# Performance work log

Hardware: AMD Instinct MI355X
Metric: run time of the kernel (lower is better)

The kernel has to match this reference:

```python
import jax, jax.numpy as jnp
import numpy as np

B, S, HIDDEN = 2, 2048, 2048
H, KVH, HD = 16, 4, 128
N_REP = H // KVH
WIN = 3  # hardcoded window_size in the module
ROPE_THETA = 10000.0


def _rope(x, cos, sin):
    # x: [b, s, h, d]; cos/sin: [s, d//2]. Pairs are consecutive elements
    # (view_as_complex on reshape(..., -1, 2)): a = even idx, b = odd idx.
    a = x[..., 0::2]
    b = x[..., 1::2]
    c = cos[None, :, None, :]
    s = sin[None, :, None, :]
    out = jnp.stack([a * c - b * s, a * s + b * c], axis=-1)  # [b,s,h,d//2,2]
    return out.reshape(x.shape)


def setup_inputs() -> dict:
    key = jax.random.key(0)
    ks = jax.random.split(key, 5)
    x = jax.random.normal(ks[0], (B, S, HIDDEN), dtype=jnp.float32)
    scale = 0.02
    wq = jax.random.normal(ks[1], (HIDDEN, H * HD), dtype=jnp.float32) * scale
    wk = jax.random.normal(ks[2], (HIDDEN, KVH * HD), dtype=jnp.float32) * scale
    wv = jax.random.normal(ks[3], (HIDDEN, KVH * HD), dtype=jnp.float32) * scale
    wo = jax.random.normal(ks[4], (H * HD, HIDDEN), dtype=jnp.float32) * scale
    # Standard RoPE angles (equivalent to the complex freqs_cis)
    inv_freq = 1.0 / (ROPE_THETA ** (np.arange(0, HD, 2, dtype=np.float64) / HD))
    ang = np.outer(np.arange(S, dtype=np.float64), inv_freq)  # [S, HD//2]
    cos = jnp.asarray(np.cos(ang), dtype=jnp.float32)
    sin = jnp.asarray(np.sin(ang), dtype=jnp.float32)
    return {"x": x, "wq": wq, "wk": wk, "wv": wv, "wo": wo, "cos": cos, "sin": sin}


def reference(x, wq, wk, wv, wo, cos, sin):
    q = (x @ wq).reshape(B, S, H, HD)
    k = (x @ wk).reshape(B, S, KVH, HD)
    v = (x @ wv).reshape(B, S, KVH, HD)
    q = _rope(q, cos, sin)
    k = _rope(k, cos, sin)
    # GQA: repeat kv heads (repeat_kv)
    k = jnp.repeat(k, N_REP, axis=2)  # [B,S,H,HD]
    v = jnp.repeat(v, N_REP, axis=2)
    scores = jnp.einsum("bqhd,bkhd->bhqk", q, k) / np.float32(np.sqrt(HD))
    i = jnp.arange(S)[:, None]
    j = jnp.arange(S)[None, :]
    allowed = (j <= i) & (j > i - WIN)
    scores = jnp.where(allowed, scores, -jnp.inf)
    attn = jax.nn.softmax(scores.astype(jnp.float32), axis=-1).astype(q.dtype)
    out = jnp.einsum("bhqk,bkhd->bqhd", attn, v).reshape(B, S, H * HD)
    return (out @ wo, attn)
```

## Files before the change

kernel.cpp:

```cpp
#include <hip/hip_runtime.h>

#define SEQ 2048
#define HID 2048
#define NH 16
#define NKVH 4
#define HDIM 128
#define NB 2
#define MTOT (NB * SEQ)
#define QKV_N (NH * HDIM + 2 * NKVH * HDIM)
#define OUT0_ELEMS (NB * SEQ * HID)
#define ATTN_ELEMS ((size_t)NB * NH * SEQ * SEQ)
#define Z1_CHUNK 26048
#define Z1_TOTAL ((long)768 * Z1_CHUNK)
#define Z2_CHUNK 26464

typedef __bf16 bf16x8 __attribute__((ext_vector_type(8)));
typedef float f32x4 __attribute__((ext_vector_type(4)));

__device__ __forceinline__ unsigned short f2bf(float f) {
  unsigned int u = __float_as_uint(f);
  u += 0x7FFFu + ((u >> 16) & 1u);
  return (unsigned short)(u >> 16);
}
__device__ __forceinline__ float bf2f(unsigned short u) {
  return __uint_as_float(((unsigned int)u) << 16);
}

__global__ __launch_bounds__(256) void prep_k(
    const float* __restrict__ x, const float* __restrict__ wq,
    const float* __restrict__ wk, const float* __restrict__ wv,
    const float* __restrict__ wo, unsigned short* __restrict__ Xbf,
    unsigned short* __restrict__ Wqkvt, unsigned short* __restrict__ Wot) {
  __shared__ float tile[32][33];
  const int bid = blockIdx.x, t = threadIdx.x;
  if (bid < 8192) {
    int i = bid * 256 + t;
    float4 v = ((const float4*)x)[i];
    ushort4 o;
    o.x = f2bf(v.x); o.y = f2bf(v.y); o.z = f2bf(v.z); o.w = f2bf(v.w);
    ((ushort4*)Xbf)[i] = o;
    return;
  }
  int lb = bid - 8192;
  const float* W; unsigned short* Wt; int gx, N;
  if (lb < 4096)      { W = wq; Wt = Wqkvt;                       gx = 64; N = 2048; }
  else if (lb < 5120) { W = wk; Wt = Wqkvt + (size_t)2048 * HID;  gx = 16; N = 512;  lb -= 4096; }
  else if (lb < 6144) { W = wv; Wt = Wqkvt + (size_t)2560 * HID;  gx = 16; N = 512;  lb -= 5120; }
  else                { W = wo; Wt = Wot;                         gx = 64; N = 2048; lb -= 6144; }
  const int n0 = (lb % gx) * 32, k0 = (lb / gx) * 32;
  const int tx = t & 31, ty = t >> 5;
  #pragma unroll
  for (int r = 0; r < 32; r += 8)
    tile[ty + r][tx] = W[(size_t)(k0 + ty + r) * N + n0 + tx];
  __syncthreads();
  #pragma unroll
  for (int r = 0; r < 32; r += 8)
    Wt[(size_t)(n0 + ty + r) * HID + k0 + tx] = f2bf(tile[tx][ty + r]);
}

template <bool OUT_BF16>
__global__ __launch_bounds__(256, 4) void gemm_bt_k(
    const unsigned short* __restrict__ A, const unsigned short* __restrict__ Bt,
    void* __restrict__ Cv, int M, int N, int K,
    f32x4* __restrict__ attn4, long zoff, int zchunk) {
  __shared__ unsigned short As[128 * 64];
  __shared__ unsigned short Bs[128 * 64];
  const int t = threadIdx.x;
  const int nbx = gridDim.x;
  const int rawbid = blockIdx.y * nbx + blockIdx.x;
  const int nwg = nbx * gridDim.y;
  const int sw = (rawbid & 7) * (nwg >> 3) + (rawbid >> 3);
  const int row0 = (sw / nbx) << 7;
  const int col0 = (sw % nbx) << 7;
  const int lane = t & 63;
  const int wave = t >> 6;
  const int wr = (wave >> 1) << 6;
  const int wc = (wave & 1) << 6;
  const int lrow = lane & 15;
  const int kofs = (lane >> 4) << 3;

  const long zbase = zoff + (long)rawbid * zchunk;

  f32x4 acc[4][4];
  #pragma unroll
  for (int a = 0; a < 4; ++a)
    #pragma unroll
    for (int b = 0; b < 4; ++b)
      #pragma unroll
      for (int r = 0; r < 4; ++r) acc[a][b][r] = 0.f;

  const unsigned short* Ab = A + (size_t)row0 * K;
  const unsigned short* Bb = Bt + (size_t)col0 * K;

  const int nk = K >> 6;
  for (int kt = 0; kt < nk; ++kt) {
    const int k0 = kt << 6;
    if (kt) __syncthreads();
    #pragma unroll
    for (int i = 0; i < 4; ++i) {
      const int c = i * 256 + t;
      const int row = c >> 3, c8 = (c & 7) << 3;
      __builtin_amdgcn_global_load_lds(
          (const __attribute__((address_space(1))) void*)(Ab + (size_t)row * K + k0 + c8),
          (__attribute__((address_space(3))) void*)(As + c * 8), 16, 0, 0);
      __builtin_amdgcn_global_load_lds(
          (const __attribute__((address_space(1))) void*)(Bb + (size_t)row * K + k0 + c8),
          (__attribute__((address_space(3))) void*)(Bs + c * 8), 16, 0, 0);
    }
    __syncthreads();

    #pragma unroll
    for (int s = 0; s < 4; ++s) {
      int il = (kt * 4 + s) * 256 + t;
      if (il < zchunk) {
        long g = zbase + il;
        int c = (int)(g & 511);
        int i = (int)((g >> 9) & (SEQ - 1));
        int hi = i >> 2;
        int lo = (i >= 2 ? i - 2 : 0) >> 2;
        if (c != hi && c != lo) {
          f32x4 z = {0.f, 0.f, 0.f, 0.f};
          __builtin_nontemporal_store(z, attn4 + g);
        }
      }
    }

    #pragma unroll
    for (int ks = 0; ks < 2; ++ks) {
      bf16x8 af[4], bfr[4];
      #pragma unroll
      for (int mf = 0; mf < 4; ++mf)
        af[mf] = *(const bf16x8*)(As + ((wr + mf * 16 + lrow) << 6) + (ks << 5) + kofs);
      #pragma unroll
      for (int nf = 0; nf < 4; ++nf)
        bfr[nf] = *(const bf16x8*)(Bs + ((wc + nf * 16 + lrow) << 6) + (ks << 5) + kofs);
      #pragma unroll
      for (int mf = 0; mf < 4; ++mf)
        #pragma unroll
        for (int nf = 0; nf < 4; ++nf)
          acc[mf][nf] = __builtin_amdgcn_mfma_f32_16x16x32_bf16(af[mf], bfr[nf],
                                                                acc[mf][nf], 0, 0, 0);
    }
  }

  const int cr = row0 + wr + ((lane >> 4) << 2);
  const int cc = col0 + wc + (lane & 15);
  #pragma unroll
  for (int mf = 0; mf < 4; ++mf)
    #pragma unroll
    for (int nf = 0; nf < 4; ++nf)
      #pragma unroll
      for (int r = 0; r < 4; ++r) {
        size_t idx = (size_t)(cr + mf * 16 + r) * N + cc + nf * 16;
        if constexpr (OUT_BF16)
          ((unsigned short*)Cv)[idx] = f2bf(acc[mf][nf][r]);
        else
          ((float*)Cv)[idx] = acc[mf][nf][r];
      }
}

__global__ void attn_k(const unsigned short* __restrict__ QKV,
                       unsigned short* __restrict__ AO,
                       float* __restrict__ attn_out,
                       const float* __restrict__ cosT,
                       const float* __restrict__ sinT) {
  int unit = blockIdx.x * 4 + (threadIdx.x >> 6);
  int lane = threadIdx.x & 63;
  int kh = unit & (NKVH - 1);
  int mi = unit >> 2;
  int i = mi & (SEQ - 1);
  int b = mi >> 11;
  const float SCALE = 0.08838834764831845f;

  float ci = cosT[i * 64 + lane], si = sinT[i * 64 + lane];

  float qa[4], qb[4];
  #pragma unroll
  for (int hh = 0; hh < 4; ++hh) {
    ushort2 qv = *(const ushort2*)(QKV + (size_t)mi * QKV_N + (kh * 4 + hh) * HDIM + 2 * lane);
    float a = bf2f(qv.x), bb = bf2f(qv.y);
    qa[hh] = a * ci - bb * si;
    qb[hh] = a * si + bb * ci;
  }

  float ka[3], kb[3], va[3], vb[3];
  #pragma unroll
  for (int jj = 0; jj < 3; ++jj) { ka[jj] = kb[jj] = va[jj] = vb[jj] = 0.f; }
  #pragma unroll
  for (int jj = 0; jj < 3; ++jj) {
    int j = i - 2 + jj;
    if (j >= 0) {
      const unsigned short* rp = QKV + (size_t)(mi - i + j) * QKV_N;
      float cj = cosT[j * 64 + lane], sj = sinT[j * 64 + lane];
      ushort2 kv = *(const ushort2*)(rp + 2048 + kh * HDIM + 2 * lane);
      float a = bf2f(kv.x), bb = bf2f(kv.y);
      ka[jj] = a * cj - bb * sj;
      kb[jj] = a * sj + bb * cj;
      ushort2 vv = *(const ushort2*)(rp + 2560 + kh * HDIM + 2 * lane);
      va[jj] = bf2f(vv.x); vb[jj] = bf2f(vv.y);
    }
  }

  float d[4][3];
  #pragma unroll
  for (int hh = 0; hh < 4; ++hh)
    #pragma unroll
    for (int jj = 0; jj < 3; ++jj) {
      int j = i - 2 + jj;
      float part = qa[hh] * ka[jj] + qb[hh] * kb[jj];
      #pragma unroll
      for (int o = 32; o; o >>= 1) part += __shfl_xor(part, o, 64);
      d[hh][jj] = (j >= 0) ? part * SCALE : -1e30f;
    }

  int rowb = (b * NH + kh * 4) * SEQ + i;
  int lo = (i >= 2 ? i - 2 : 0) >> 2;
  int hi = i >> 2;
  #pragma unroll
  for (int hh = 0; hh < 4; ++hh) {
    float mx = fmaxf(fmaxf(d[hh][0], d[hh][1]), d[hh][2]);
    float p0 = __expf(d[hh][0] - mx), p1 = __expf(d[hh][1] - mx), p2 = __expf(d[hh][2] - mx);
    float inv = 1.0f / (p0 + p1 + p2);
    float aw0 = p0 * inv, aw1 = p1 * inv, aw2 = p2 * inv;

    float oa = aw0 * va[0] + aw1 * va[1] + aw2 * va[2];
    float ob = aw0 * vb[0] + aw1 * vb[1] + aw2 * vb[2];
    ushort2 ov; ov.x = f2bf(oa); ov.y = f2bf(ob);
    *(ushort2*)(AO + (size_t)mi * HID + (kh * 4 + hh) * HDIM + 2 * lane) = ov;

    if (lane == 2 * hh || (lane == 2 * hh + 1 && hi != lo)) {
      int c = (lane == 2 * hh) ? lo : hi;
      f32x4 val = {0.f, 0.f, 0.f, 0.f};
      float aw[3] = {aw0, aw1, aw2};
      #pragma unroll
      for (int q = 0; q < 4; ++q) {
        int j = c * 4 + q;
        int dd = j - (i - 2);
        if (dd >= 0 && dd < 3 && j <= i) val[q] = aw[dd];
      }
      __builtin_nontemporal_store(
          val, (f32x4*)(attn_out + ((size_t)rowb + (size_t)hh * SEQ) * SEQ) + c);
    }
  }
}

extern "C" void kernel_launch(void* const* d_in, const int* in_sizes, int n_in,
                              void* d_out, int out_size, void* d_ws, size_t ws_size,
                              hipStream_t stream) {
  const float* x    = (const float*)d_in[0];
  const float* wq   = (const float*)d_in[1];
  const float* wk   = (const float*)d_in[2];
  const float* wv   = (const float*)d_in[3];
  const float* wo   = (const float*)d_in[4];
  const float* cosT = (const float*)d_in[5];
  const float* sinT = (const float*)d_in[6];

  float* out  = (float*)d_out;
  float* attn = out + OUT0_ELEMS;

  char* ws = (char*)d_ws;
  unsigned short* Xbf   = (unsigned short*)ws;  ws += (size_t)MTOT * HID * 2;
  unsigned short* Wqkvt = (unsigned short*)ws;  ws += (size_t)QKV_N * HID * 2;
  unsigned short* Wot   = (unsigned short*)ws;  ws += (size_t)HID * HID * 2;
  unsigned short* QKV   = (unsigned short*)ws;  ws += (size_t)MTOT * QKV_N * 2;
  unsigned short* AO    = (unsigned short*)ws;

  prep_k<<<18432, 256, 0, stream>>>(x, wq, wk, wv, wo, Xbf, Wqkvt, Wot);

  gemm_bt_k<true><<<dim3(QKV_N / 128, MTOT / 128), 256, 0, stream>>>(
      Xbf, Wqkvt, QKV, MTOT, QKV_N, HID, (f32x4*)attn, 0L, Z1_CHUNK);

  attn_k<<<MTOT * NKVH / 4, 256, 0, stream>>>(QKV, AO, attn, cosT, sinT);

  gemm_bt_k<false><<<dim3(HID / 128, MTOT / 128), 256, 0, stream>>>(
      AO, Wot, out, MTOT, HID, HID, (f32x4*)attn, Z1_TOTAL, Z2_CHUNK);
}
```

Baseline: 188.8 us.

## Move Wo transpose and part of attn zero-fill into attention kernel

```diff
diff --git a/kernel.cpp b/kernel.cpp
--- a/kernel.cpp
+++ b/kernel.cpp
@@ -10,7 +10,9 @@
 #define QKV_N (NH * HDIM + 2 * NKVH * HDIM)
 #define OUT0_ELEMS (NB * SEQ * HID)
 #define ATTN_ELEMS ((size_t)NB * NH * SEQ * SEQ)
-#define Z1_CHUNK 26048
+#define ZA_CHUNK 768
+#define ZA_TOTAL ((long)4096 * ZA_CHUNK)
+#define Z1_CHUNK 21952
 #define Z1_TOTAL ((long)768 * Z1_CHUNK)
 #define Z2_CHUNK 26464
 
@@ -29,8 +31,7 @@
 __global__ __launch_bounds__(256) void prep_k(
     const float* __restrict__ x, const float* __restrict__ wq,
     const float* __restrict__ wk, const float* __restrict__ wv,
-    const float* __restrict__ wo, unsigned short* __restrict__ Xbf,
-    unsigned short* __restrict__ Wqkvt, unsigned short* __restrict__ Wot) {
+    unsigned short* __restrict__ Xbf, unsigned short* __restrict__ Wqkvt) {
   __shared__ float tile[32][33];
   const int bid = blockIdx.x, t = threadIdx.x;
   if (bid < 8192) {
@@ -45,8 +46,7 @@
   const float* W; unsigned short* Wt; int gx, N;
   if (lb < 4096)      { W = wq; Wt = Wqkvt;                       gx = 64; N = 2048; }
   else if (lb < 5120) { W = wk; Wt = Wqkvt + (size_t)2048 * HID;  gx = 16; N = 512;  lb -= 4096; }
-  else if (lb < 6144) { W = wv; Wt = Wqkvt + (size_t)2560 * HID;  gx = 16; N = 512;  lb -= 5120; }
-  else                { W = wo; Wt = Wot;                         gx = 64; N = 2048; lb -= 6144; }
+  else                { W = wv; Wt = Wqkvt + (size_t)2560 * HID;  gx = 16; N = 512;  lb -= 5120; }
   const int n0 = (lb % gx) * 32, k0 = (lb / gx) * 32;
   const int tx = t & 31, ty = t >> 5;
   #pragma unroll
@@ -163,9 +163,41 @@
                        unsigned short* __restrict__ AO,
                        float* __restrict__ attn_out,
                        const float* __restrict__ cosT,
-                       const float* __restrict__ sinT) {
-  int unit = blockIdx.x * 4 + (threadIdx.x >> 6);
-  int lane = threadIdx.x & 63;
+                       const float* __restrict__ sinT,
+                       const float* __restrict__ wo,
+                       unsigned short* __restrict__ Wot) {
+  __shared__ float tile[32][33];
+  const int bid = blockIdx.x, t = threadIdx.x;
+
+  if (bid >= 4096) {
+    int lb = bid - 4096;
+    const int n0 = (lb & 63) * 32, k0 = (lb >> 6) * 32;
+    const int tx = t & 31, ty = t >> 5;
+    #pragma unroll
+    for (int r = 0; r < 32; r += 8)
+      tile[ty + r][tx] = wo[(size_t)(k0 + ty + r) * HID + n0 + tx];
+    __syncthreads();
+    #pragma unroll
+    for (int r = 0; r < 32; r += 8)
+      Wot[(size_t)(n0 + ty + r) * HID + k0 + tx] = f2bf(tile[tx][ty + r]);
+    return;
+  }
+
+  #pragma unroll
+  for (int s = 0; s < 3; ++s) {
+    long g = (long)bid * ZA_CHUNK + s * 256 + t;
+    int c = (int)(g & 511);
+    int qi = (int)((g >> 9) & (SEQ - 1));
+    int zhi = qi >> 2;
+    int zlo = (qi >= 2 ? qi - 2 : 0) >> 2;
+    if (c != zhi && c != zlo) {
+      f32x4 z = {0.f, 0.f, 0.f, 0.f};
+      __builtin_nontemporal_store(z, (f32x4*)attn_out + g);
+    }
+  }
+
+  int unit = bid * 4 + (t >> 6);
+  int lane = t & 63;
   int kh = unit & (NKVH - 1);
   int mi = unit >> 2;
   int i = mi & (SEQ - 1);
@@ -265,13 +297,13 @@
   unsigned short* QKV   = (unsigned short*)ws;  ws += (size_t)MTOT * QKV_N * 2;
   unsigned short* AO    = (unsigned short*)ws;
 
-  prep_k<<<18432, 256, 0, stream>>>(x, wq, wk, wv, wo, Xbf, Wqkvt, Wot);
+  prep_k<<<14336, 256, 0, stream>>>(x, wq, wk, wv, Xbf, Wqkvt);
 
   gemm_bt_k<true><<<dim3(QKV_N / 128, MTOT / 128), 256, 0, stream>>>(
-      Xbf, Wqkvt, QKV, MTOT, QKV_N, HID, (f32x4*)attn, 0L, Z1_CHUNK);
-
-  attn_k<<<MTOT * NKVH / 4, 256, 0, stream>>>(QKV, AO, attn, cosT, sinT);
+      Xbf, Wqkvt, QKV, MTOT, QKV_N, HID, (f32x4*)attn, ZA_TOTAL, Z1_CHUNK);
+
+  attn_k<<<8192, 256, 0, stream>>>(QKV, AO, attn, cosT, sinT, wo, Wot);
 
   gemm_bt_k<false><<<dim3(HID / 128, MTOT / 128), 256, 0, stream>>>(
-      AO, Wot, out, MTOT, HID, HID, (f32x4*)attn, Z1_TOTAL, Z2_CHUNK);
-}
+      AO, Wot, out, MTOT, HID, HID, (f32x4*)attn, ZA_TOTAL + Z1_TOTAL, Z2_CHUNK);
+}
```

New measurement: 185.8 us, median of 2. No clear change (-1.6%).
